# Kernel optimization log

Hardware: AMD Instinct MI355X
Metric: run time of the kernel (lower is better)

Reference implementation:

```python
import jax, jax.numpy as jnp
import numpy as np

INPUT_SIZE = 1
HIDDEN = 20


def setup_inputs() -> dict:
    key = jax.random.key(0)
    ks = jax.random.split(key, 7)
    B, S = 4096, 512
    scale = 1.0 / np.sqrt(HIDDEN)  # torch LSTM/Linear init range
    x = jax.random.normal(ks[0], (B, S, INPUT_SIZE), dtype=jnp.float32)
    W_ih = jax.random.uniform(ks[1], (4 * HIDDEN, INPUT_SIZE), jnp.float32, -scale, scale)
    W_hh = jax.random.uniform(ks[2], (4 * HIDDEN, HIDDEN), jnp.float32, -scale, scale)
    b_ih = jax.random.uniform(ks[3], (4 * HIDDEN,), jnp.float32, -scale, scale)
    b_hh = jax.random.uniform(ks[4], (4 * HIDDEN,), jnp.float32, -scale, scale)
    W_lin = jax.random.uniform(ks[5], (1, HIDDEN), jnp.float32, -scale, scale)
    b_lin = jax.random.uniform(ks[6], (1,), jnp.float32, -scale, scale)
    return {"x": x, "W_ih": W_ih, "W_hh": W_hh, "b_ih": b_ih,
            "b_hh": b_hh, "W_lin": W_lin, "b_lin": b_lin}


def _lstm_seq(x, W_ih, W_hh, b_ih, b_hh):
    # x: [B, S, 1]; returns all hidden states [B, S, H]
    B = x.shape[0]
    # precompute input contribution for all timesteps: [S, B, 4H]
    xg = jnp.einsum('bsi,gi->sbg', x, W_ih) + (b_ih + b_hh)
    h0 = jnp.zeros((B, HIDDEN), x.dtype)
    c0 = jnp.zeros((B, HIDDEN), x.dtype)

    def step(carry, xg_t):
        h, c = carry
        gates = xg_t + h @ W_hh.T  # [B, 4H]
        i, f, g, o = jnp.split(gates, 4, axis=-1)  # torch gate order: i,f,g,o
        i = jax.nn.sigmoid(i)
        f = jax.nn.sigmoid(f)
        g = jnp.tanh(g)
        o = jax.nn.sigmoid(o)
        c_new = f * c + i * g
        h_new = o * jnp.tanh(c_new)
        return (h_new, c_new), h_new

    _, hs = jax.lax.scan(step, (h0, c0), xg)  # hs: [S, B, H]
    return jnp.transpose(hs, (1, 0, 2))  # [B, S, H]


def reference(x, W_ih, W_hh, b_ih, b_hh, W_lin, b_lin):
    h = _lstm_seq(x, W_ih, W_hh, b_ih, b_hh)  # [B, S, H]
    return h @ W_lin.T + b_lin  # [B, S, 1]
```

## Files before the change

kernel.cpp:

```cpp
#include <hip/hip_runtime.h>


#define BATCH 4096
#define SLEN  512
#define H     20
#define CHUNK 16
#define LOG2E 1.44269504088896340736f
#define GSTRIDE 200
#define RSTRIDE 12

typedef _Float16 h2 __attribute__((ext_vector_type(2)));

__device__ __forceinline__ float fexp2(float x) { return __builtin_amdgcn_exp2f(x); }
__device__ __forceinline__ float frcp(float x)  { return __builtin_amdgcn_rcpf(x); }
__device__ __forceinline__ h2 bch2(unsigned int u) { return __builtin_bit_cast(h2, u); }

__global__ __launch_bounds__(64, 2) void lstm_fused(
    const float* __restrict__ x,
    const float* __restrict__ W_ih,
    const float* __restrict__ W_hh,
    const float* __restrict__ b_ih,
    const float* __restrict__ b_hh,
    const float* __restrict__ W_lin,
    const float* __restrict__ b_lin,
    float* __restrict__ out)
{
    __shared__ __align__(16) unsigned int hw[3 * GSTRIDE];
    __shared__ float xbuf[3][CHUNK];
    _Float16* hh = (_Float16*)hw;

    const int lane = threadIdx.x;
    int grp = lane / H;
    if (grp > 2) grp = 2;
    const int j    = lane - grp * H;
    const bool valid = (grp < 2);
    const long b  = (long)blockIdx.x * 2 + grp;
    const long bc = valid ? b : 0;

    const float s1 = -LOG2E;
    const float s2 = -2.0f * LOG2E;

    const int ju = (j < H) ? j : 0;
    h2 w2[4][10];
    float bb[4], xw[4];
#pragma unroll
    for (int g = 0; g < 4; ++g) {
        const int row = g * H + ju;
        const float sc = (g == 2) ? s2 : s1;
#pragma unroll
        for (int k = 0; k < 10; ++k) {
            h2 t;
            t.x = (_Float16)(sc * W_hh[row * H + 2 * k]);
            t.y = (_Float16)(sc * W_hh[row * H + 2 * k + 1]);
            w2[g][k] = t;
        }
        bb[g] = sc * (b_ih[row] + b_hh[row]);
        xw[g] = sc * W_ih[row];
    }
    h2 wl2[10];
#pragma unroll
    for (int k = 0; k < 10; ++k) {
        h2 t;
        t.x = (_Float16)W_lin[2 * k];
        t.y = (_Float16)W_lin[2 * k + 1];
        wl2[k] = t;
    }
    const float blin = b_lin[0];

    const float* xb = x + bc * SLEN;
    float*       ob = out + bc * SLEN;

    const int gbase = grp * GSTRIDE;
    hh[2 * (gbase + (CHUNK - 1) * RSTRIDE) + ju] = (_Float16)0.0f;
    float c = 0.0f;

#pragma unroll 1
    for (int T = 0; T < SLEN; T += CHUNK) {
        if (j < CHUNK) xbuf[grp][j] = xb[T + j];

#pragma unroll
        for (int i = 0; i < CHUNK; ++i) {
            const int rp = (i + CHUNK - 1) & (CHUNK - 1);
            const int base = gbase + rp * RSTRIDE;
            const float xt = xbuf[grp][i];
            const uint4 A = *(const uint4*)&hw[base];
            const uint4 B = *(const uint4*)&hw[base + 4];
            const uint2 C2 = *(const uint2*)&hw[base + 8];
            const unsigned int pw[10] = {A.x, A.y, A.z, A.w,
                                         B.x, B.y, B.z, B.w, C2.x, C2.y};
            float a[4];
#pragma unroll
            for (int g = 0; g < 4; ++g) a[g] = fmaf(xt, xw[g], bb[g]);
#pragma unroll
            for (int k = 0; k < 10; ++k)
#pragma unroll
                for (int g = 0; g < 4; ++g)
                    a[g] = __builtin_amdgcn_fdot2(bch2(pw[k]), w2[g][k], a[g], false);

            const float eI = fexp2(a[0]);
            const float eF = fexp2(a[1]);
            const float eG = fexp2(a[2]);
            const float eO = fexp2(a[3]);
            const float pF = 1.0f + eF;
            const float P  = (1.0f + eI) * (1.0f + eG);
            const float num = fmaf(c, P, (1.0f - eG) * pF);
            c = fmaxf(num * frcp(pF * P), -34.0f);
            const float eC = fexp2(s2 * c);
            const float hval = (1.0f - eC) * frcp((1.0f + eO) * (1.0f + eC));
            hh[2 * (gbase + i * RSTRIDE) + ju] = (_Float16)hval;
        }

        if (j < CHUNK) {
            const int rb = gbase + j * RSTRIDE;
            const uint4 A = *(const uint4*)&hw[rb];
            const uint4 B = *(const uint4*)&hw[rb + 4];
            const uint2 C2 = *(const uint2*)&hw[rb + 8];
            const unsigned int pw[10] = {A.x, A.y, A.z, A.w,
                                         B.x, B.y, B.z, B.w, C2.x, C2.y};
            float y = blin;
#pragma unroll
            for (int k = 0; k < 10; ++k)
                y = __builtin_amdgcn_fdot2(bch2(pw[k]), wl2[k], y, false);
            if (valid) ob[T + j] = y;
        }
    }
}

extern "C" void kernel_launch(void* const* d_in, const int* in_sizes, int n_in,
                              void* d_out, int out_size, void* d_ws, size_t ws_size,
                              hipStream_t stream) {
    const float* x     = (const float*)d_in[0];
    const float* W_ih  = (const float*)d_in[1];
    const float* W_hh  = (const float*)d_in[2];
    const float* b_ih  = (const float*)d_in[3];
    const float* b_hh  = (const float*)d_in[4];
    const float* W_lin = (const float*)d_in[5];
    const float* b_lin = (const float*)d_in[6];
    float* out = (float*)d_out;

    const int nblocks = BATCH / 2;
    lstm_fused<<<nblocks, 64, 0, stream>>>(x, W_ih, W_hh, b_ih, b_hh,
                                           W_lin, b_lin, out);
}
```

Measured before the change: 227.3 us.

## Exchange hidden state via lane swizzle and bpermute instead of LDS rows

The recurrent hidden-state exchange now stays in registers. Each lane packs its fp16 h with its neighbour's using ds_swizzle, and the gate computation gathers the ten packed pairs with ds_bpermute, replacing the per-step LDS vector reads of the previous row. The gate dot products are also split into two accumulator chains to shorten the serial fdot2 dependency. The aim is a shorter per-timestep critical path, but it costs ten bpermute operations per step instead of three wide LDS loads. The LDS writes are kept for the output projection.

```diff
diff --git a/kernel.cpp b/kernel.cpp
--- a/kernel.cpp
+++ b/kernel.cpp
@@ -67,11 +67,15 @@
     }
     const float blin = b_lin[0];
 
+    int idx[10];
+#pragma unroll
+    for (int m = 0; m < 10; ++m) idx[m] = (grp * H + 2 * m) * 4;
+
     const float* xb = x + bc * SLEN;
     float*       ob = out + bc * SLEN;
 
     const int gbase = grp * GSTRIDE;
-    hh[2 * (gbase + (CHUNK - 1) * RSTRIDE) + ju] = (_Float16)0.0f;
+    unsigned word = 0u;
     float c = 0.0f;
 
 #pragma unroll 1
@@ -80,22 +84,30 @@
 
 #pragma unroll
         for (int i = 0; i < CHUNK; ++i) {
-            const int rp = (i + CHUNK - 1) & (CHUNK - 1);
-            const int base = gbase + rp * RSTRIDE;
+            unsigned pw[10];
+#pragma unroll
+            for (int m = 0; m < 10; ++m)
+                pw[m] = (unsigned)__builtin_amdgcn_ds_bpermute(idx[m], (int)word);
+
             const float xt = xbuf[grp][i];
-            const uint4 A = *(const uint4*)&hw[base];
-            const uint4 B = *(const uint4*)&hw[base + 4];
-            const uint2 C2 = *(const uint2*)&hw[base + 8];
-            const unsigned int pw[10] = {A.x, A.y, A.z, A.w,
-                                         B.x, B.y, B.z, B.w, C2.x, C2.y};
-            float a[4];
+            float a[4], a2[4];
 #pragma unroll
             for (int g = 0; g < 4; ++g) a[g] = fmaf(xt, xw[g], bb[g]);
 #pragma unroll
-            for (int k = 0; k < 10; ++k)
+            for (int k = 0; k < 5; ++k)
 #pragma unroll
                 for (int g = 0; g < 4; ++g)
                     a[g] = __builtin_amdgcn_fdot2(bch2(pw[k]), w2[g][k], a[g], false);
+#pragma unroll
+            for (int g = 0; g < 4; ++g)
+                a2[g] = __builtin_amdgcn_fdot2(bch2(pw[5]), w2[g][5], 0.0f, false);
+#pragma unroll
+            for (int k = 6; k < 10; ++k)
+#pragma unroll
+                for (int g = 0; g < 4; ++g)
+                    a2[g] = __builtin_amdgcn_fdot2(bch2(pw[k]), w2[g][k], a2[g], false);
+#pragma unroll
+            for (int g = 0; g < 4; ++g) a[g] += a2[g];
 
             const float eI = fexp2(a[0]);
             const float eF = fexp2(a[1]);
@@ -107,7 +119,13 @@
             c = fmaxf(num * frcp(pF * P), -34.0f);
             const float eC = fexp2(s2 * c);
             const float hval = (1.0f - eC) * frcp((1.0f + eO) * (1.0f + eC));
-            hh[2 * (gbase + i * RSTRIDE) + ju] = (_Float16)hval;
+
+            const _Float16 hf = (_Float16)hval;
+            hh[2 * (gbase + i * RSTRIDE) + j] = hf;
+
+            const unsigned own = (unsigned)__builtin_bit_cast(unsigned short, hf);
+            const int nb = __builtin_amdgcn_ds_swizzle((int)own, 0x041F);
+            word = own | ((unsigned)nb << 16);
         }
 
         if (j < CHUNK) {
@@ -115,12 +133,12 @@
             const uint4 A = *(const uint4*)&hw[rb];
             const uint4 B = *(const uint4*)&hw[rb + 4];
             const uint2 C2 = *(const uint2*)&hw[rb + 8];
-            const unsigned int pw[10] = {A.x, A.y, A.z, A.w,
-                                         B.x, B.y, B.z, B.w, C2.x, C2.y};
+            const unsigned int pwh[10] = {A.x, A.y, A.z, A.w,
+                                          B.x, B.y, B.z, B.w, C2.x, C2.y};
             float y = blin;
 #pragma unroll
             for (int k = 0; k < 10; ++k)
-                y = __builtin_amdgcn_fdot2(bch2(pw[k]), wl2[k], y, false);
+                y = __builtin_amdgcn_fdot2(bch2(pwh[k]), wl2[k], y, false);
             if (valid) ob[T + j] = y;
         }
     }
```

Result: slower. 274.0 us (+20.6%).
